# Kernel optimization log

Measured on AMD Instinct MI355X. Metric: run time of the kernel, lower is better.

Reference implementation:

```python
import jax, jax.numpy as jnp
import numpy as np

N_NODES = 50000
N_EDGES = 800000
D_FEAT = 128
EMBED = 128


def setup_inputs() -> dict:
    key = jax.random.key(0)
    ks = jax.random.split(key, 6)
    node_features = jax.random.normal(ks[0], (N_NODES, D_FEAT), dtype=jnp.float32)
    senders = jax.random.randint(ks[1], (N_EDGES,), 0, N_NODES, dtype=jnp.int32)
    receivers = jax.random.randint(ks[2], (N_EDGES,), 0, N_NODES, dtype=jnp.int32)
    edge_features = jax.random.normal(ks[3], (N_EDGES, D_FEAT), dtype=jnp.float32)
    # xavier-normal-ish scaled params
    W = jax.random.normal(ks[4], (D_FEAT, 2 * EMBED), dtype=jnp.float32) * (2.0 / (D_FEAT + 2 * EMBED)) ** 0.5
    W_e = jax.random.normal(ks[5], (D_FEAT, EMBED), dtype=jnp.float32) * (2.0 / (D_FEAT + EMBED)) ** 0.5
    b_W = jnp.zeros((2 * EMBED,), dtype=jnp.float32)
    b_We = jnp.zeros((EMBED,), dtype=jnp.float32)
    return dict(node_features=node_features, senders=senders, receivers=receivers,
                edge_features=edge_features, W=W, b_W=b_W, W_e=W_e, b_We=b_We)


def reference(node_features, senders, receivers, edge_features, W, b_W, W_e, b_We):
    num_nodes = node_features.shape[-2]
    # dense proj then split into self (xi) and neighbor (xj) halves
    h = node_features @ W + b_W              # [N, 2*E]
    xi, xj = jnp.split(h, 2, axis=-1)        # [N, E] each
    # gather neighbor messages per edge
    xji = xj[senders]                         # [E, E]
    xji = xji + (edge_features @ W_e + b_We)  # edge feature contribution
    # degree normalization
    in_degree = jax.ops.segment_sum(jnp.ones_like(receivers, dtype=xji.dtype), receivers, num_segments=num_nodes)
    xji = xji / (in_degree[receivers][..., None] + 1e-6)
    nodes = xi + jax.ops.segment_sum(xji, receivers, num_segments=num_nodes)
    return nodes
```

## Files before the change

### kernel.cpp

```cpp
#include <hip/hip_runtime.h>

#define NN 50000
#define NE 800000
#define DF 128
#define BM 32
#define NB ((NN + BM - 1) / BM)
#define SCAN_B ((NN + 255) / 256)
#define GB ((NN + 63) / 64)
#define HB ((NE + 255) / 256)

typedef __attribute__((ext_vector_type(8))) short bf16x8;
typedef __attribute__((ext_vector_type(4))) float f32x4;

static const size_t OFF_DEG  = 0;
static const size_t OFF_OFFS = 204800;
static const size_t OFF_PART = 409600;
static const size_t OFF_RANK = 614400;
static const size_t OFF_CSR  = 3814400;
static const size_t OFF_WT   = 10214400;
static const size_t OFF_WET  = 10279936;
static const size_t OFF_P1   = 10312704;
static const size_t OFF_P2   = 35937280;

__device__ __forceinline__ unsigned f2bf(float f) {
    unsigned u = __float_as_uint(f);
    return (u + 0x7FFFu + ((u >> 16) & 1u)) >> 16;
}

__global__ void k_setup(const float* __restrict__ W, const float* __restrict__ We,
                        unsigned* __restrict__ deg, unsigned short* __restrict__ Wt,
                        unsigned short* __restrict__ WeT) {
    int idx = blockIdx.x * blockDim.x + threadIdx.x;
    if (idx < NN) deg[idx] = 0;
    if (idx < 256 * 128) {
        int n = idx >> 7, k = idx & 127;
        Wt[idx] = (unsigned short)f2bf(W[k * 256 + n]);
    }
    if (idx < 128 * 128) {
        int n = idx >> 7, k = idx & 127;
        WeT[idx] = (unsigned short)f2bf(We[k * 128 + n]);
    }
}

__global__ __launch_bounds__(256) void k_gemm1hist(
    const float* __restrict__ X, const unsigned short* __restrict__ Wt,
    float* __restrict__ P1, unsigned short* __restrict__ P2,
    const int* __restrict__ rcv, unsigned* __restrict__ deg,
    unsigned* __restrict__ rank) {
    __shared__ unsigned short As[64 * 128];
    if (blockIdx.x >= GB) {
        int e = (blockIdx.x - GB) * 256 + threadIdx.x;
        if (e < NE) rank[e] = atomicAdd(&deg[rcv[e]], 1u);
        return;
    }
    const int tid = threadIdx.x;
    const int w = tid >> 6, lane = tid & 63;
    const int l15 = lane & 15, l4 = lane >> 4;
    const int m0 = blockIdx.x * 64;
    char* Asb = (char*)As;

    for (int i = tid; i < 64 * 32; i += 256) {
        int r = i >> 5, g = i & 31;
        int n = m0 + r;
        f32x4 v = {0.f, 0.f, 0.f, 0.f};
        if (n < NN) v = *reinterpret_cast<const f32x4*>(X + (size_t)n * DF + g * 4);
        unsigned pk0 = f2bf(v[0]) | (f2bf(v[1]) << 16);
        unsigned pk1 = f2bf(v[2]) | (f2bf(v[3]) << 16);
        unsigned byte = (unsigned)(r * 256 + g * 8) ^ ((unsigned)(r & 7) << 4);
        *reinterpret_cast<uint2*>(Asb + byte) = make_uint2(pk0, pk1);
    }
    __syncthreads();

    const int rrow = w * 16 + l15;
    const unsigned rswz = (unsigned)(rrow & 7) << 4;
    f32x4 acc[16];
#pragma unroll
    for (int ng = 0; ng < 16; ++ng) acc[ng] = (f32x4){0.f, 0.f, 0.f, 0.f};
#pragma unroll
    for (int kk = 0; kk < 4; ++kk) {
        unsigned abyte = (unsigned)(rrow * 256 + (kk * 32 + l4 * 8) * 2) ^ rswz;
        bf16x8 a = *reinterpret_cast<const bf16x8*>(Asb + abyte);
#pragma unroll
        for (int ng = 0; ng < 16; ++ng) {
            bf16x8 b = *reinterpret_cast<const bf16x8*>(
                Wt + (size_t)(ng * 16 + l15) * 128 + kk * 32 + l4 * 8);
            acc[ng] = __builtin_amdgcn_mfma_f32_16x16x32_bf16(a, b, acc[ng], 0, 0, 0);
        }
    }
#pragma unroll
    for (int ng = 0; ng < 16; ++ng) {
        int col = ng * 16 + l15;
#pragma unroll
        for (int j = 0; j < 4; ++j) {
            int row = m0 + w * 16 + l4 * 4 + j;
            if (row < NN) {
                if (col < 128) P1[(size_t)row * DF + col] = acc[ng][j];
                else P2[(size_t)row * DF + (col - 128)] = (unsigned short)f2bf(acc[ng][j]);
            }
        }
    }
}

__global__ void k_scan1(const unsigned* __restrict__ deg, unsigned* __restrict__ part) {
    int idx = blockIdx.x * 256 + threadIdx.x;
    unsigned v = (idx < NN) ? deg[idx] : 0;
#pragma unroll
    for (int o = 32; o; o >>= 1) v += __shfl_down(v, o);
    __shared__ unsigned wsum[4];
    int w = threadIdx.x >> 6, lane = threadIdx.x & 63;
    if (lane == 0) wsum[w] = v;
    __syncthreads();
    if (threadIdx.x == 0) part[blockIdx.x] = wsum[0] + wsum[1] + wsum[2] + wsum[3];
}

__global__ void k_scan2(unsigned* __restrict__ part, unsigned* __restrict__ offs) {
    __shared__ unsigned sh[SCAN_B];
    int t = threadIdx.x;
    if (t < SCAN_B) sh[t] = part[t];
    __syncthreads();
    if (t == 0) {
        unsigned run = 0;
        for (int i = 0; i < SCAN_B; ++i) { unsigned v = sh[i]; sh[i] = run; run += v; }
        offs[NN] = run;
    }
    __syncthreads();
    if (t < SCAN_B) part[t] = sh[t];
}

__global__ void k_scan3(const unsigned* __restrict__ deg, const unsigned* __restrict__ part,
                        unsigned* __restrict__ offs) {
    int idx = blockIdx.x * 256 + threadIdx.x;
    unsigned v = (idx < NN) ? deg[idx] : 0;
    int w = threadIdx.x >> 6, lane = threadIdx.x & 63;
    unsigned x = v;
#pragma unroll
    for (int o = 1; o < 64; o <<= 1) {
        unsigned y = __shfl_up(x, o);
        if (lane >= o) x += y;
    }
    __shared__ unsigned wsum[4];
    if (lane == 63) wsum[w] = x;
    __syncthreads();
    unsigned base = part[blockIdx.x];
    for (int i = 0; i < w; ++i) base += wsum[i];
    if (idx < NN) offs[idx] = base + x - v;
}

__global__ void k_scatter(const int* __restrict__ snd, const int* __restrict__ rcv,
                          const unsigned* __restrict__ offs, const unsigned* __restrict__ rank,
                          int2* __restrict__ csr) {
    int e = blockIdx.x * blockDim.x + threadIdx.x;
    if (e >= NE) return;
    csr[offs[rcv[e]] + rank[e]] = make_int2(snd[e], e);
}

__global__ __launch_bounds__(512) void k_aggemm(
    const float* __restrict__ EF, const unsigned short* __restrict__ P2,
    const float* __restrict__ P1, const unsigned* __restrict__ offs,
    const int2* __restrict__ csr, const unsigned short* __restrict__ WeT,
    const float* __restrict__ bW, const float* __restrict__ bWe,
    float* __restrict__ out) {
    __shared__ unsigned short AeS[BM * 128];
    __shared__ float XJ[BM][128];
    __shared__ float cf_s[BM];
    const int tid = threadIdx.x;
    const int w = tid >> 6, lane = tid & 63;
    const int m0 = blockIdx.x * BM;
    char* Asb = (char*)AeS;

    {
        const int q = lane >> 4;
        const int l15 = lane & 15;
        const int cA = l15 * 4;
        const int cP = l15 * 8;
        for (int t = 0; t < 4; ++t) {
            int r = w * 4 + t;
            int n = m0 + r;
            unsigned s0 = 0, s1 = 0;
            if (n < NN) { s0 = offs[n]; s1 = offs[n + 1]; }
            s0 = __builtin_amdgcn_readfirstlane(s0);
            s1 = __builtin_amdgcn_readfirstlane(s1);
            unsigned dg = s1 - s0;
            f32x4 ef0 = {0.f,0.f,0.f,0.f}, ef1 = {0.f,0.f,0.f,0.f};
            f32x4 xj0 = {0.f,0.f,0.f,0.f}, xj1 = {0.f,0.f,0.f,0.f};
            unsigned trips = (dg + 3) >> 2;
            unsigned p = s0 + q;
#pragma unroll 2
            for (unsigned it = 0; it < trips; ++it, p += 4) {
                bool act = p < s1;
                unsigned pc = act ? p : s0;
                int2 se = csr[pc];
                const float* er = EF + (size_t)se.y * DF;
                f32x4 e0 = *reinterpret_cast<const f32x4*>(er + cA);
                f32x4 e1 = *reinterpret_cast<const f32x4*>(er + 64 + cA);
                uint4 pu = *reinterpret_cast<const uint4*>(P2 + (size_t)se.x * DF + cP);
                float m = act ? 1.f : 0.f;
                ef0 += m * e0; ef1 += m * e1;
                xj0[0] += m * __uint_as_float(pu.x << 16);
                xj0[1] += m * __uint_as_float(pu.x & 0xFFFF0000u);
                xj0[2] += m * __uint_as_float(pu.y << 16);
                xj0[3] += m * __uint_as_float(pu.y & 0xFFFF0000u);
                xj1[0] += m * __uint_as_float(pu.z << 16);
                xj1[1] += m * __uint_as_float(pu.z & 0xFFFF0000u);
                xj1[2] += m * __uint_as_float(pu.w << 16);
                xj1[3] += m * __uint_as_float(pu.w & 0xFFFF0000u);
            }
#pragma unroll
            for (int i = 0; i < 4; ++i) {
                ef0[i] += __shfl_xor(ef0[i], 16); ef0[i] += __shfl_xor(ef0[i], 32);
                ef1[i] += __shfl_xor(ef1[i], 16); ef1[i] += __shfl_xor(ef1[i], 32);
                xj0[i] += __shfl_xor(xj0[i], 16); xj0[i] += __shfl_xor(xj0[i], 32);
                xj1[i] += __shfl_xor(xj1[i], 16); xj1[i] += __shfl_xor(xj1[i], 32);
            }
            float inv = 1.0f / ((float)dg + 1e-6f);
            unsigned swz = (unsigned)(r & 7) << 4;
            if (q == 0) {
                ef0 *= inv; ef1 *= inv;
                unsigned b0 = (unsigned)(r * 256 + cA * 2) ^ swz;
                unsigned b1 = (unsigned)(r * 256 + (64 + cA) * 2) ^ swz;
                *reinterpret_cast<uint2*>(Asb + b0) =
                    make_uint2(f2bf(ef0[0]) | (f2bf(ef0[1]) << 16),
                               f2bf(ef0[2]) | (f2bf(ef0[3]) << 16));
                *reinterpret_cast<uint2*>(Asb + b1) =
                    make_uint2(f2bf(ef1[0]) | (f2bf(ef1[1]) << 16),
                               f2bf(ef1[2]) | (f2bf(ef1[3]) << 16));
            } else if (q == 1) {
                xj0 *= inv; xj1 *= inv;
                *reinterpret_cast<f32x4*>(&XJ[r][cP]) = xj0;
                *reinterpret_cast<f32x4*>(&XJ[r][cP + 4]) = xj1;
            }
            if (lane == 0) cf_s[r] = (float)dg * inv;
        }
    }
    __syncthreads();

    {
        const int l15 = lane & 15, l4 = lane >> 4;
        const int h = w & 1;
        const int rrow = h * 16 + l15;
        const int n0 = (w >> 1) * 32;
        f32x4 acc[2];
        acc[0] = (f32x4){0.f, 0.f, 0.f, 0.f};
        acc[1] = (f32x4){0.f, 0.f, 0.f, 0.f};
        const unsigned rswz = (unsigned)(rrow & 7) << 4;
#pragma unroll
        for (int kk = 0; kk < 4; ++kk) {
            unsigned abyte = (unsigned)(rrow * 256 + (kk * 32 + l4 * 8) * 2) ^ rswz;
            bf16x8 a = *reinterpret_cast<const bf16x8*>(Asb + abyte);
            bf16x8 b0 = *reinterpret_cast<const bf16x8*>(
                WeT + (size_t)(n0 + l15) * 128 + kk * 32 + l4 * 8);
            bf16x8 b1 = *reinterpret_cast<const bf16x8*>(
                WeT + (size_t)(n0 + 16 + l15) * 128 + kk * 32 + l4 * 8);
            acc[0] = __builtin_amdgcn_mfma_f32_16x16x32_bf16(a, b0, acc[0], 0, 0, 0);
            acc[1] = __builtin_amdgcn_mfma_f32_16x16x32_bf16(a, b1, acc[1], 0, 0, 0);
        }
#pragma unroll
        for (int ng = 0; ng < 2; ++ng) {
            int col = n0 + ng * 16 + l15;
            float bx = bW[col];
            float bj = bW[128 + col] + bWe[col];
#pragma unroll
            for (int j = 0; j < 4; ++j) {
                int lr = h * 16 + l4 * 4 + j;
                int row = m0 + lr;
                if (row < NN)
                    out[(size_t)row * DF + col] =
                        P1[(size_t)row * DF + col] + XJ[lr][col] +
                        acc[ng][j] + bx + cf_s[lr] * bj;
            }
        }
    }
}

extern "C" void kernel_launch(void* const* d_in, const int* in_sizes, int n_in,
                              void* d_out, int out_size, void* d_ws, size_t ws_size,
                              hipStream_t stream) {
    const float* X   = (const float*)d_in[0];
    const int*   snd = (const int*)d_in[1];
    const int*   rcv = (const int*)d_in[2];
    const float* EF  = (const float*)d_in[3];
    const float* W   = (const float*)d_in[4];
    const float* bW  = (const float*)d_in[5];
    const float* We  = (const float*)d_in[6];
    const float* bWe = (const float*)d_in[7];
    float* out = (float*)d_out;

    char* ws = (char*)d_ws;
    unsigned* deg  = (unsigned*)(ws + OFF_DEG);
    unsigned* offs = (unsigned*)(ws + OFF_OFFS);
    unsigned* part = (unsigned*)(ws + OFF_PART);
    unsigned* rank = (unsigned*)(ws + OFF_RANK);
    int2*     csr  = (int2*)(ws + OFF_CSR);
    unsigned short* Wt  = (unsigned short*)(ws + OFF_WT);
    unsigned short* WeT = (unsigned short*)(ws + OFF_WET);
    float*          P1  = (float*)(ws + OFF_P1);
    unsigned short* P2  = (unsigned short*)(ws + OFF_P2);

    k_setup<<<(NN + 255) / 256, 256, 0, stream>>>(W, We, deg, Wt, WeT);
    k_gemm1hist<<<GB + HB, 256, 0, stream>>>(X, Wt, P1, P2, rcv, deg, rank);
    k_scan1<<<SCAN_B, 256, 0, stream>>>(deg, part);
    k_scan2<<<1, 256, 0, stream>>>(part, offs);
    k_scan3<<<SCAN_B, 256, 0, stream>>>(deg, part, offs);
    k_scatter<<<(NE + 255) / 256, 256, 0, stream>>>(snd, rcv, offs, rank, csr);
    k_aggemm<<<NB, 512, 0, stream>>>(EF, P2, P1, offs, csr, WeT, bW, bWe, out);
}
```

Measured before the change: 238.7 us.

## Fuse self projection into edge GEMM via concatenated K and drop P1 buffer

The xi = X·W[:, :128] projection moves out of the first GEMM and into the aggregation kernel. It is computed there as one K=256 MFMA GEMM over the concatenated [X | mean edge features] tile against a stacked weight matrix. This removes the fp32 P1 round trip, a 25.6 MB write and read, and halves the first GEMM. The edge gather loop is also rewritten so each lane handles 2 columns per edge sequentially, instead of 4 edges in parallel with shuffle reductions. That gives narrower per-lane loads and longer serial dependency chains per node.

```diff
diff --git a/kernel.cpp b/kernel.cpp
--- a/kernel.cpp
+++ b/kernel.cpp
@@ -17,10 +17,9 @@
 static const size_t OFF_PART = 409600;
 static const size_t OFF_RANK = 614400;
 static const size_t OFF_CSR  = 3814400;
-static const size_t OFF_WT   = 10214400;
-static const size_t OFF_WET  = 10279936;
-static const size_t OFF_P1   = 10312704;
-static const size_t OFF_P2   = 35937280;
+static const size_t OFF_BCTA = 10214400;
+static const size_t OFF_W2T  = 10279936;
+static const size_t OFF_P2   = 10312704;
 
 __device__ __forceinline__ unsigned f2bf(float f) {
     unsigned u = __float_as_uint(f);
@@ -28,25 +27,25 @@
 }
 
 __global__ void k_setup(const float* __restrict__ W, const float* __restrict__ We,
-                        unsigned* __restrict__ deg, unsigned short* __restrict__ Wt,
-                        unsigned short* __restrict__ WeT) {
+                        unsigned* __restrict__ deg, unsigned short* __restrict__ BcTa,
+                        unsigned short* __restrict__ W2T) {
     int idx = blockIdx.x * blockDim.x + threadIdx.x;
     if (idx < NN) deg[idx] = 0;
-    if (idx < 256 * 128) {
-        int n = idx >> 7, k = idx & 127;
-        Wt[idx] = (unsigned short)f2bf(W[k * 256 + n]);
+    if (idx < 128 * 256) {
+        int col = idx >> 8, k = idx & 255;
+        float v = (k < 128) ? W[k * 256 + col] : We[(k - 128) * 128 + col];
+        BcTa[idx] = (unsigned short)f2bf(v);
     }
     if (idx < 128 * 128) {
-        int n = idx >> 7, k = idx & 127;
-        WeT[idx] = (unsigned short)f2bf(We[k * 128 + n]);
+        int col = idx >> 7, k = idx & 127;
+        W2T[idx] = (unsigned short)f2bf(W[k * 256 + 128 + col]);
     }
 }
 
 __global__ __launch_bounds__(256) void k_gemm1hist(
-    const float* __restrict__ X, const unsigned short* __restrict__ Wt,
-    float* __restrict__ P1, unsigned short* __restrict__ P2,
-    const int* __restrict__ rcv, unsigned* __restrict__ deg,
-    unsigned* __restrict__ rank) {
+    const float* __restrict__ X, const unsigned short* __restrict__ W2T,
+    unsigned short* __restrict__ P2, const int* __restrict__ rcv,
+    unsigned* __restrict__ deg, unsigned* __restrict__ rank) {
     __shared__ unsigned short As[64 * 128];
     if (blockIdx.x >= GB) {
         int e = (blockIdx.x - GB) * 256 + threadIdx.x;
@@ -73,30 +72,27 @@
 
     const int rrow = w * 16 + l15;
     const unsigned rswz = (unsigned)(rrow & 7) << 4;
-    f32x4 acc[16];
-#pragma unroll
-    for (int ng = 0; ng < 16; ++ng) acc[ng] = (f32x4){0.f, 0.f, 0.f, 0.f};
+    f32x4 acc[8];
+#pragma unroll
+    for (int ng = 0; ng < 8; ++ng) acc[ng] = (f32x4){0.f, 0.f, 0.f, 0.f};
 #pragma unroll
     for (int kk = 0; kk < 4; ++kk) {
         unsigned abyte = (unsigned)(rrow * 256 + (kk * 32 + l4 * 8) * 2) ^ rswz;
         bf16x8 a = *reinterpret_cast<const bf16x8*>(Asb + abyte);
 #pragma unroll
-        for (int ng = 0; ng < 16; ++ng) {
+        for (int ng = 0; ng < 8; ++ng) {
             bf16x8 b = *reinterpret_cast<const bf16x8*>(
-                Wt + (size_t)(ng * 16 + l15) * 128 + kk * 32 + l4 * 8);
+                W2T + (size_t)(ng * 16 + l15) * 128 + kk * 32 + l4 * 8);
             acc[ng] = __builtin_amdgcn_mfma_f32_16x16x32_bf16(a, b, acc[ng], 0, 0, 0);
         }
     }
 #pragma unroll
-    for (int ng = 0; ng < 16; ++ng) {
+    for (int ng = 0; ng < 8; ++ng) {
         int col = ng * 16 + l15;
 #pragma unroll
         for (int j = 0; j < 4; ++j) {
             int row = m0 + w * 16 + l4 * 4 + j;
-            if (row < NN) {
-                if (col < 128) P1[(size_t)row * DF + col] = acc[ng][j];
-                else P2[(size_t)row * DF + (col - 128)] = (unsigned short)f2bf(acc[ng][j]);
-            }
+            if (row < NN) P2[(size_t)row * DF + col] = (unsigned short)f2bf(acc[ng][j]);
         }
     }
 }
@@ -155,24 +151,32 @@
 }
 
 __global__ __launch_bounds__(512) void k_aggemm(
-    const float* __restrict__ EF, const unsigned short* __restrict__ P2,
-    const float* __restrict__ P1, const unsigned* __restrict__ offs,
-    const int2* __restrict__ csr, const unsigned short* __restrict__ WeT,
+    const float* __restrict__ X, const float* __restrict__ EF,
+    const unsigned short* __restrict__ P2, const unsigned* __restrict__ offs,
+    const int2* __restrict__ csr, const unsigned short* __restrict__ BcTa,
     const float* __restrict__ bW, const float* __restrict__ bWe,
     float* __restrict__ out) {
-    __shared__ unsigned short AeS[BM * 128];
+    __shared__ unsigned short As[BM * 256];
     __shared__ float XJ[BM][128];
     __shared__ float cf_s[BM];
     const int tid = threadIdx.x;
     const int w = tid >> 6, lane = tid & 63;
     const int m0 = blockIdx.x * BM;
-    char* Asb = (char*)AeS;
+    char* Asb = (char*)As;
+
+    for (int i = tid; i < BM * 32; i += 512) {
+        int r = i >> 5, g = i & 31;
+        int n = m0 + r;
+        f32x4 v = {0.f, 0.f, 0.f, 0.f};
+        if (n < NN) v = *reinterpret_cast<const f32x4*>(X + (size_t)n * DF + g * 4);
+        unsigned pk0 = f2bf(v[0]) | (f2bf(v[1]) << 16);
+        unsigned pk1 = f2bf(v[2]) | (f2bf(v[3]) << 16);
+        unsigned byte = (unsigned)(r * 512 + g * 8) ^ ((unsigned)(r & 7) << 4);
+        *reinterpret_cast<uint2*>(Asb + byte) = make_uint2(pk0, pk1);
+    }
 
     {
-        const int q = lane >> 4;
-        const int l15 = lane & 15;
-        const int cA = l15 * 4;
-        const int cP = l15 * 8;
+        const int l2 = lane * 2;
         for (int t = 0; t < 4; ++t) {
             int r = w * 4 + t;
             int n = m0 + r;
@@ -180,56 +184,23 @@
             if (n < NN) { s0 = offs[n]; s1 = offs[n + 1]; }
             s0 = __builtin_amdgcn_readfirstlane(s0);
             s1 = __builtin_amdgcn_readfirstlane(s1);
-            unsigned dg = s1 - s0;
-            f32x4 ef0 = {0.f,0.f,0.f,0.f}, ef1 = {0.f,0.f,0.f,0.f};
-            f32x4 xj0 = {0.f,0.f,0.f,0.f}, xj1 = {0.f,0.f,0.f,0.f};
-            unsigned trips = (dg + 3) >> 2;
-            unsigned p = s0 + q;
-#pragma unroll 2
-            for (unsigned it = 0; it < trips; ++it, p += 4) {
-                bool act = p < s1;
-                unsigned pc = act ? p : s0;
-                int2 se = csr[pc];
-                const float* er = EF + (size_t)se.y * DF;
-                f32x4 e0 = *reinterpret_cast<const f32x4*>(er + cA);
-                f32x4 e1 = *reinterpret_cast<const f32x4*>(er + 64 + cA);
-                uint4 pu = *reinterpret_cast<const uint4*>(P2 + (size_t)se.x * DF + cP);
-                float m = act ? 1.f : 0.f;
-                ef0 += m * e0; ef1 += m * e1;
-                xj0[0] += m * __uint_as_float(pu.x << 16);
-                xj0[1] += m * __uint_as_float(pu.x & 0xFFFF0000u);
-                xj0[2] += m * __uint_as_float(pu.y << 16);
-                xj0[3] += m * __uint_as_float(pu.y & 0xFFFF0000u);
-                xj1[0] += m * __uint_as_float(pu.z << 16);
-                xj1[1] += m * __uint_as_float(pu.z & 0xFFFF0000u);
-                xj1[2] += m * __uint_as_float(pu.w << 16);
-                xj1[3] += m * __uint_as_float(pu.w & 0xFFFF0000u);
+            float efa = 0.f, efb = 0.f, xja = 0.f, xjb = 0.f;
+#pragma unroll 8
+            for (unsigned p = s0; p < s1; ++p) {
+                int2 se = csr[p];
+                float2 ev = *reinterpret_cast<const float2*>(EF + (size_t)se.y * DF + l2);
+                unsigned pu = *reinterpret_cast<const unsigned*>(P2 + (size_t)se.x * DF + l2);
+                efa += ev.x; efb += ev.y;
+                xja += __uint_as_float(pu << 16);
+                xjb += __uint_as_float(pu & 0xFFFF0000u);
             }
-#pragma unroll
-            for (int i = 0; i < 4; ++i) {
-                ef0[i] += __shfl_xor(ef0[i], 16); ef0[i] += __shfl_xor(ef0[i], 32);
-                ef1[i] += __shfl_xor(ef1[i], 16); ef1[i] += __shfl_xor(ef1[i], 32);
-                xj0[i] += __shfl_xor(xj0[i], 16); xj0[i] += __shfl_xor(xj0[i], 32);
-                xj1[i] += __shfl_xor(xj1[i], 16); xj1[i] += __shfl_xor(xj1[i], 32);
-            }
-            float inv = 1.0f / ((float)dg + 1e-6f);
-            unsigned swz = (unsigned)(r & 7) << 4;
-            if (q == 0) {
-                ef0 *= inv; ef1 *= inv;
-                unsigned b0 = (unsigned)(r * 256 + cA * 2) ^ swz;
-                unsigned b1 = (unsigned)(r * 256 + (64 + cA) * 2) ^ swz;
-                *reinterpret_cast<uint2*>(Asb + b0) =
-                    make_uint2(f2bf(ef0[0]) | (f2bf(ef0[1]) << 16),
-                               f2bf(ef0[2]) | (f2bf(ef0[3]) << 16));
-                *reinterpret_cast<uint2*>(Asb + b1) =
-                    make_uint2(f2bf(ef1[0]) | (f2bf(ef1[1]) << 16),
-                               f2bf(ef1[2]) | (f2bf(ef1[3]) << 16));
-            } else if (q == 1) {
-                xj0 *= inv; xj1 *= inv;
-                *reinterpret_cast<f32x4*>(&XJ[r][cP]) = xj0;
-                *reinterpret_cast<f32x4*>(&XJ[r][cP + 4]) = xj1;
-            }
-            if (lane == 0) cf_s[r] = (float)dg * inv;
+            float dg = (float)(s1 - s0);
+            float inv = 1.0f / (dg + 1e-6f);
+            unsigned pk = f2bf(efa * inv) | (f2bf(efb * inv) << 16);
+            unsigned byte = (unsigned)(r * 512 + 256 + lane * 4) ^ ((unsigned)(r & 7) << 4);
+            *reinterpret_cast<unsigned*>(Asb + byte) = pk;
+            *reinterpret_cast<float2*>(&XJ[r][l2]) = make_float2(xja * inv, xjb * inv);
+            if (lane == 0) cf_s[r] = dg * inv;
         }
     }
     __syncthreads();
@@ -239,34 +210,32 @@
         const int h = w & 1;
         const int rrow = h * 16 + l15;
         const int n0 = (w >> 1) * 32;
-        f32x4 acc[2];
-        acc[0] = (f32x4){0.f, 0.f, 0.f, 0.f};
-        acc[1] = (f32x4){0.f, 0.f, 0.f, 0.f};
+        f32x4 acc0 = {0.f, 0.f, 0.f, 0.f}, acc1 = {0.f, 0.f, 0.f, 0.f};
         const unsigned rswz = (unsigned)(rrow & 7) << 4;
 #pragma unroll
-        for (int kk = 0; kk < 4; ++kk) {
-            unsigned abyte = (unsigned)(rrow * 256 + (kk * 32 + l4 * 8) * 2) ^ rswz;
+        for (int kk = 0; kk < 8; ++kk) {
+            unsigned abyte = (unsigned)(rrow * 512 + (kk * 32 + l4 * 8) * 2) ^ rswz;
             bf16x8 a = *reinterpret_cast<const bf16x8*>(Asb + abyte);
             bf16x8 b0 = *reinterpret_cast<const bf16x8*>(
-                WeT + (size_t)(n0 + l15) * 128 + kk * 32 + l4 * 8);
+                BcTa + (size_t)(n0 + l15) * 256 + kk * 32 + l4 * 8);
             bf16x8 b1 = *reinterpret_cast<const bf16x8*>(
-                WeT + (size_t)(n0 + 16 + l15) * 128 + kk * 32 + l4 * 8);
-            acc[0] = __builtin_amdgcn_mfma_f32_16x16x32_bf16(a, b0, acc[0], 0, 0, 0);
-            acc[1] = __builtin_amdgcn_mfma_f32_16x16x32_bf16(a, b1, acc[1], 0, 0, 0);
+                BcTa + (size_t)(n0 + 16 + l15) * 256 + kk * 32 + l4 * 8);
+            acc0 = __builtin_amdgcn_mfma_f32_16x16x32_bf16(a, b0, acc0, 0, 0, 0);
+            acc1 = __builtin_amdgcn_mfma_f32_16x16x32_bf16(a, b1, acc1, 0, 0, 0);
         }
 #pragma unroll
         for (int ng = 0; ng < 2; ++ng) {
             int col = n0 + ng * 16 + l15;
             float bx = bW[col];
             float bj = bW[128 + col] + bWe[col];
+            f32x4 acc = ng ? acc1 : acc0;
 #pragma unroll
             for (int j = 0; j < 4; ++j) {
                 int lr = h * 16 + l4 * 4 + j;
                 int row = m0 + lr;
                 if (row < NN)
                     out[(size_t)row * DF + col] =
-                        P1[(size_t)row * DF + col] + XJ[lr][col] +
-                        acc[ng][j] + bx + cf_s[lr] * bj;
+                        acc[j] + XJ[lr][col] + bx + cf_s[lr] * bj;
             }
         }
     }
@@ -291,16 +260,15 @@
     unsigned* part = (unsigned*)(ws + OFF_PART);
     unsigned* rank = (unsigned*)(ws + OFF_RANK);
     int2*     csr  = (int2*)(ws + OFF_CSR);
-    unsigned short* Wt  = (unsigned short*)(ws + OFF_WT);
-    unsigned short* WeT = (unsigned short*)(ws + OFF_WET);
-    float*          P1  = (float*)(ws + OFF_P1);
-    unsigned short* P2  = (unsigned short*)(ws + OFF_P2);
-
-    k_setup<<<(NN + 255) / 256, 256, 0, stream>>>(W, We, deg, Wt, WeT);
-    k_gemm1hist<<<GB + HB, 256, 0, stream>>>(X, Wt, P1, P2, rcv, deg, rank);
+    unsigned short* BcTa = (unsigned short*)(ws + OFF_BCTA);
+    unsigned short* W2T  = (unsigned short*)(ws + OFF_W2T);
+    unsigned short* P2   = (unsigned short*)(ws + OFF_P2);
+
+    k_setup<<<(NN + 255) / 256, 256, 0, stream>>>(W, We, deg, BcTa, W2T);
+    k_gemm1hist<<<GB + HB, 256, 0, stream>>>(X, W2T, P2, rcv, deg, rank);
     k_scan1<<<SCAN_B, 256, 0, stream>>>(deg, part);
     k_scan2<<<1, 256, 0, stream>>>(part, offs);
     k_scan3<<<SCAN_B, 256, 0, stream>>>(deg, part, offs);
     k_scatter<<<(NE + 255) / 256, 256, 0, stream>>>(snd, rcv, offs, rank, csr);
-    k_aggemm<<<NB, 512, 0, stream>>>(EF, P2, P1, offs, csr, WeT, bW, bWe, out);
-}
+    k_aggemm<<<NB, 512, 0, stream>>>(X, EF, P2, offs, csr, BcTa, bW, bWe, out);
+}
```

Measured after the change: 212.7 us. 10.9% less time.
